# Optimization experiments

Measured on AMD Instinct MI355X. Metric: run time of the kernel, lower is better.

Reference implementation:

```python
import jax, jax.numpy as jnp
import numpy as np

SIGMA = 0.05
KSIZE = 3
MIN_VAL = 50.0
MAX_VAL = 100.0


def _gauss_kernel():
    # ax = range(-(3//2)+1, 3//2+1) = [-1, 0, 1]  (matches TF int-floor-div)
    ax = jnp.arange(-(KSIZE // 2) + 1.0, KSIZE // 2 + 1.0)
    xx, yy = jnp.meshgrid(ax, ax)
    k = jnp.exp(-(xx ** 2 + yy ** 2) / (2.0 * SIGMA ** 2))
    k = k / jnp.sum(k)
    return k[..., None, None].astype(jnp.float32)  # HWIO, C=1


def _reflect_pad(x):
    return jnp.pad(x, ((0, 0), (1, 1), (1, 1), (0, 0)), mode='reflect')


def _conv(x, k):
    return jax.lax.conv_general_dilated(x, k, (1, 1), 'VALID',
                                        dimension_numbers=('NHWC', 'HWIO', 'NHWC'))


def _canny(images):
    blur = _conv(_reflect_pad(images), _gauss_kernel())
    h = jnp.array([[-1, 0, 1], [-2, 0, 2], [-1, 0, 1]], jnp.float32)[..., None, None]
    v = jnp.array([[-1, -2, -1], [0, 0, 0], [1, 2, 1]], jnp.float32)[..., None, None]
    bp = _reflect_pad(blur)
    gx = _conv(bp, h)
    gy = _conv(bp, v)
    gxy = jnp.sqrt(gx ** 2 + gy ** 2)
    # NOTE: original uses atan2(gx, gy) in this arg order
    theta = (jnp.arctan2(gx, gy) * (180.0 / np.pi) + 90.0) % 180.0

    H, W = gx.shape[1], gx.shape[2]
    # dilation2d with a -inf/0 kernel == max over the kernel's zero-offsets of the
    # zero-padded image; offsets are (dy,dx) of the 0 entries of each 3x3 filter.
    offsets = [
        [(1, 0), (1, 1), (1, 2)],  # horizontal bin: middle row
        [(0, 2), (1, 1), (2, 0)],  # 45 deg: anti-diagonal
        [(0, 1), (1, 1), (2, 1)],  # vertical bin: middle column
        [(0, 0), (1, 1), (2, 2)],  # 135 deg: main diagonal
    ]
    conds = [
        jnp.logical_or(theta >= 157.5, theta < 22.5),
        jnp.logical_and(theta >= 22.5, theta < 67.5),
        jnp.logical_and(theta >= 67.5, theta < 112.5),
        jnp.logical_and(theta >= 112.5, theta < 157.5),
    ]

    edge = jnp.zeros_like(gxy)
    for cond, offs in zip(conds, offsets):
        ang = jnp.where(cond, gxy, 0.0)
        pad = jnp.pad(ang, ((0, 0), (1, 1), (1, 1), (0, 0)))  # zero pad, as ZeroPadding2D
        mp = pad[:, offs[0][0]:offs[0][0] + H, offs[0][1]:offs[0][1] + W, :]
        for dy, dx in offs[1:]:
            mp = jnp.maximum(mp, pad[:, dy:dy + H, dx:dx + W, :])
        edge = edge + jnp.where(mp == ang, ang, 0.0)

    edge_sure = jnp.where(edge >= MAX_VAL, 255.0, 0.0)
    edge_week = jnp.where(jnp.logical_and(edge >= MIN_VAL, edge < MAX_VAL), 255.0, 0.0)
    edge_image = jnp.where(jnp.logical_or(edge_week == 255.0, edge_sure == 255.0), 255.5, 0.0)
    return edge_image, edge_week, edge_sure


def setup_inputs() -> dict:
    key = jax.random.key(0)
    images = jax.random.uniform(key, (16, 1024, 1024, 1), dtype=jnp.float32) * 255.0
    return {"images": images}


def reference(images):
    return _canny(images)
```

## Files before the change

kernel.cpp:

```cpp
#include <hip/hip_runtime.h>
#include <math.h>

#define IMG_H 1024
#define IMG_W 1024
#define OUT_H 1025
#define OUT_W 1025
#define NIMG  16
#define TOTAL (NIMG * OUT_H * OUT_W)

#define TILE_W 64
#define TILE_H 16
#define HALO_W 68
#define HALO_H 18
#define NQX    17
#define NQUAD  (HALO_H * NQX)
#define NTHREADS 320

__device__ __forceinline__ int refl(int k) {
    if (k >= 2) return (k <= 1025) ? (k - 2) : 1022;
    return k;
}

__device__ __forceinline__ void sobel_generic(const float* __restrict__ img, int i, int j,
                                              float& gx, float& gy) {
    int r0 = refl(i), r1 = refl(i + 1), r2 = refl(i + 2);
    int c0 = refl(j), c1 = refl(j + 1), c2 = refl(j + 2);
    const float* p0 = img + r0 * IMG_W;
    const float* p1 = img + r1 * IMG_W;
    const float* p2 = img + r2 * IMG_W;
    float v00 = p0[c0], v01 = p0[c1], v02 = p0[c2];
    float v10 = p1[c0],               v12 = p1[c2];
    float v20 = p2[c0], v21 = p2[c1], v22 = p2[c2];

    float t = -v00;
    t = __fadd_rn(t, v02);
    t = __fadd_rn(t, -2.0f * v10);
    t = __fadd_rn(t, 2.0f * v12);
    t = __fadd_rn(t, -v20);
    gx = __fadd_rn(t, v22);

    t = -v00;
    t = __fadd_rn(t, -2.0f * v01);
    t = __fadd_rn(t, -v02);
    t = __fadd_rn(t, v20);
    t = __fadd_rn(t, 2.0f * v21);
    gy = __fadd_rn(t, v22);
}

__device__ int classify_slow(float gx, float gy) {
    float t = (float)atan2((double)gx, (double)gy);
    float deg = __fmul_rn(t, (float)(180.0 / M_PI));
    float th = __fadd_rn(deg, 90.0f);
    th = fmodf(th, 180.0f);
    if (th < 0.0f) th += 180.0f;
    if (th < 22.5f || th >= 157.5f) return 0;
    if (th < 67.5f) return 1;
    if (th < 112.5f) return 2;
    return 3;
}

__device__ __forceinline__ int classify(float gx, float gy) {
    float ax = fabsf(gx), ay = fabsf(gy);
    const float T22_LO = 0.414172141e0f;
    const float T22_HI = 0.414254984e0f;
    const float T67_LO = 2.413972141e0f;
    const float T67_HI = 2.414454984e0f;

    if (ax <= ay * T22_LO) return 2;
    if (ax >= ay * T67_HI) return 0;
    if (ax >= ay * T22_HI && ax <= ay * T67_LO) {
        unsigned s = (__float_as_uint(gx) ^ __float_as_uint(gy)) >> 31;
        return s ? 1 : 3;
    }
    return classify_slow(gx, gy);
}

__device__ __forceinline__ float mag(float gx, float gy) {
    return __fsqrt_rn(__fadd_rn(__fmul_rn(gx, gx), __fmul_rn(gy, gy)));
}

__device__ __forceinline__ void load6(const float* __restrict__ p, float v[6]) {
    float4 a = *(const float4*)p;
    float2 b = *(const float2*)(p + 4);
    v[0] = a.x; v[1] = a.y; v[2] = a.z; v[3] = a.w; v[4] = b.x; v[5] = b.y;
}

__global__ __launch_bounds__(NTHREADS) void canny_kernel(const float* __restrict__ images,
                                                         float* __restrict__ out) {
    __shared__ float    g_s[HALO_H * HALO_W];
    __shared__ unsigned b_u[HALO_H * NQX];

    const int tile_ox = blockIdx.x * TILE_W;
    const int tile_oy = blockIdx.y * TILE_H;
    const int n       = blockIdx.z;
    const float* img = images + (size_t)n * IMG_H * IMG_W;
    const int t = threadIdx.x;

    if (t < NQUAD) {
        int hy  = t / NQX;
        int qx  = t - hy * NQX;
        int oy  = tile_oy + hy - 1;
        int ox0 = tile_ox + qx * 4 - 2;

        float    gq[4];
        unsigned bq[4];

        if (oy >= 2 && oy <= 1023 && ox0 >= 2 && ox0 <= 1020) {
            const float* r0p = img + (oy - 2) * IMG_W + (ox0 - 2);
            float R0[6], R1[6], R2[6];
            load6(r0p, R0);
            load6(r0p + IMG_W, R1);
            load6(r0p + 2 * IMG_W, R2);
            #pragma unroll
            for (int p = 0; p < 4; p++) {
                float v00 = R0[p], v01 = R0[p + 1], v02 = R0[p + 2];
                float v10 = R1[p],                  v12 = R1[p + 2];
                float v20 = R2[p], v21 = R2[p + 1], v22 = R2[p + 2];

                float s = -v00;
                s = __fadd_rn(s, v02);
                s = __fadd_rn(s, -2.0f * v10);
                s = __fadd_rn(s, 2.0f * v12);
                s = __fadd_rn(s, -v20);
                float gx = __fadd_rn(s, v22);

                s = -v00;
                s = __fadd_rn(s, -2.0f * v01);
                s = __fadd_rn(s, -v02);
                s = __fadd_rn(s, v20);
                s = __fadd_rn(s, 2.0f * v21);
                float gy = __fadd_rn(s, v22);

                gq[p] = mag(gx, gy);
                bq[p] = (unsigned)classify(gx, gy);
            }
        } else {
            #pragma unroll
            for (int p = 0; p < 4; p++) {
                int ox = ox0 + p;
                float g = -1.0f;
                unsigned b = 255u;
                if (oy >= 0 && oy < OUT_H && ox >= 0 && ox < OUT_W) {
                    float gx, gy;
                    sobel_generic(img, oy, ox, gx, gy);
                    g = mag(gx, gy);
                    b = (unsigned)classify(gx, gy);
                }
                gq[p] = g;
                bq[p] = b;
            }
        }

        int ldoff = hy * HALO_W + qx * 4;
        *(float4*)&g_s[ldoff] = make_float4(gq[0], gq[1], gq[2], gq[3]);
        b_u[hy * NQX + qx] = bq[0] | (bq[1] << 8) | (bq[2] << 16) | (bq[3] << 24);
    }
    __syncthreads();

    const unsigned char* b_s = (const unsigned char*)b_u;
    #pragma unroll
    for (int q = 0; q < 4; q++) {
        int p = t + NTHREADS * q;
        if (p >= TILE_W * TILE_H) break;
        int r = p >> 6, c = p & 63;
        int oy = tile_oy + r, ox = tile_ox + c;
        if (oy >= OUT_H || ox >= OUT_W) continue;

        int hc = (r + 1) * HALO_W + (c + 2);
        float gc = g_s[hc];
        int   bc = b_s[hc];

        int doff = (bc == 0) ? 1
                 : (bc == 1) ? (HALO_W - 1)
                 : (bc == 2) ? HALO_W
                 :             (HALO_W + 1);

        float nmax = 0.0f;
        float g1 = g_s[hc + doff];
        if (b_s[hc + doff] == bc && g1 > nmax) nmax = g1;
        float g2 = g_s[hc - doff];
        if (b_s[hc - doff] == bc && g2 > nmax) nmax = g2;

        float e = (gc >= nmax) ? gc : 0.0f;

        size_t o = (size_t)(n * OUT_H + oy) * OUT_W + ox;
        out[o]                       = (e >= 50.0f) ? 255.5f : 0.0f;
        out[(size_t)TOTAL + o]       = (e >= 50.0f && e < 100.0f) ? 255.0f : 0.0f;
        out[(size_t)(2 * TOTAL) + o] = (e >= 100.0f) ? 255.0f : 0.0f;
    }
}

extern "C" void kernel_launch(void* const* d_in, const int* in_sizes, int n_in,
                              void* d_out, int out_size, void* d_ws, size_t ws_size,
                              hipStream_t stream) {
    const float* images = (const float*)d_in[0];
    float* out = (float*)d_out;
    dim3 grid((OUT_W + TILE_W - 1) / TILE_W,
              (OUT_H + TILE_H - 1) / TILE_H,
              NIMG);
    canny_kernel<<<grid, NTHREADS, 0, stream>>>(images, out);
}
```

Before: 301.7 us.

## Replace 2D tiles with per-wave vertical strip streaming and LDS ring buffer

Replaces the 2D tiled block (halo gradient computed into shared memory, then a block-wide sync) with a per-wavefront column strip that walks down a band of rows. Input rows are prefetched into registers, and gradient magnitude and direction bins go into a 4-row LDS ring buffer that is private to each wave. This removes the __syncthreads and the halo recomputation between vertically adjacent tiles. In exchange it adds a serial dependency along rows within each wave, uses narrower per-lane scalar loads instead of float4 loads, and has 2 of every 64 lanes doing halo-only work.

```diff
diff --git a/kernel.cpp b/kernel.cpp
--- a/kernel.cpp
+++ b/kernel.cpp
@@ -8,43 +8,24 @@
 #define NIMG  16
 #define TOTAL (NIMG * OUT_H * OUT_W)
 
-#define TILE_W 64
-#define TILE_H 16
-#define HALO_W 68
-#define HALO_H 18
-#define NQX    17
-#define NQUAD  (HALO_H * NQX)
-#define NTHREADS 320
+#define STRIPW   62
+#define NSTRIPS  17
+#define NBANDS   16
+#define BANDH    65
+#define WAVES_PER_BLOCK 4
+#define NTHREADS 256
+#define NWAVES  (NSTRIPS * NBANDS * NIMG)
+#define NBLOCKS (NWAVES / WAVES_PER_BLOCK)
 
-__device__ __forceinline__ int refl(int k) {
+#define GR_W 68
+#define LDS_PER_WAVE_DW (2 * 4 * GR_W)
+
+__device__ __forceinline__ int refl_idx(int k) {
     if (k >= 2) return (k <= 1025) ? (k - 2) : 1022;
     return k;
 }
-
-__device__ __forceinline__ void sobel_generic(const float* __restrict__ img, int i, int j,
-                                              float& gx, float& gy) {
-    int r0 = refl(i), r1 = refl(i + 1), r2 = refl(i + 2);
-    int c0 = refl(j), c1 = refl(j + 1), c2 = refl(j + 2);
-    const float* p0 = img + r0 * IMG_W;
-    const float* p1 = img + r1 * IMG_W;
-    const float* p2 = img + r2 * IMG_W;
-    float v00 = p0[c0], v01 = p0[c1], v02 = p0[c2];
-    float v10 = p1[c0],               v12 = p1[c2];
-    float v20 = p2[c0], v21 = p2[c1], v22 = p2[c2];
-
-    float t = -v00;
-    t = __fadd_rn(t, v02);
-    t = __fadd_rn(t, -2.0f * v10);
-    t = __fadd_rn(t, 2.0f * v12);
-    t = __fadd_rn(t, -v20);
-    gx = __fadd_rn(t, v22);
-
-    t = -v00;
-    t = __fadd_rn(t, -2.0f * v01);
-    t = __fadd_rn(t, -v02);
-    t = __fadd_rn(t, v20);
-    t = __fadd_rn(t, 2.0f * v21);
-    gy = __fadd_rn(t, v22);
+__device__ __forceinline__ int clamp0(int k, int hi) {
+    return k < 0 ? 0 : (k > hi ? hi : k);
 }
 
 __device__ int classify_slow(float gx, float gy) {
@@ -79,43 +60,66 @@
     return __fsqrt_rn(__fadd_rn(__fmul_rn(gx, gx), __fmul_rn(gy, gy)));
 }
 
-__device__ __forceinline__ void load6(const float* __restrict__ p, float v[6]) {
-    float4 a = *(const float4*)p;
-    float2 b = *(const float2*)(p + 4);
-    v[0] = a.x; v[1] = a.y; v[2] = a.z; v[3] = a.w; v[4] = b.x; v[5] = b.y;
-}
+__global__ __launch_bounds__(NTHREADS, 5) void canny_kernel(const float* __restrict__ images,
+                                                            float* __restrict__ out) {
+    __shared__ float lds[WAVES_PER_BLOCK * LDS_PER_WAVE_DW];
 
-__global__ __launch_bounds__(NTHREADS) void canny_kernel(const float* __restrict__ images,
-                                                         float* __restrict__ out) {
-    __shared__ float    g_s[HALO_H * HALO_W];
-    __shared__ unsigned b_u[HALO_H * NQX];
+    const int tid = threadIdx.x;
+    const int w   = tid >> 6;
+    const int L   = tid & 63;
 
-    const int tile_ox = blockIdx.x * TILE_W;
-    const int tile_oy = blockIdx.y * TILE_H;
-    const int n       = blockIdx.z;
-    const float* img = images + (size_t)n * IMG_H * IMG_W;
-    const int t = threadIdx.x;
+    const int gw    = blockIdx.x * WAVES_PER_BLOCK + w;
+    const int img_i = gw / (NSTRIPS * NBANDS);
+    const int rem   = gw - img_i * (NSTRIPS * NBANDS);
+    const int band  = rem / NSTRIPS;
+    const int strip = rem - band * NSTRIPS;
 
-    if (t < NQUAD) {
-        int hy  = t / NQX;
-        int qx  = t - hy * NQX;
-        int oy  = tile_oy + hy - 1;
-        int ox0 = tile_ox + qx * 4 - 2;
+    const float* img = images + (size_t)img_i * IMG_H * IMG_W;
 
-        float    gq[4];
-        unsigned bq[4];
+    const int col0 = strip * STRIPW;
+    const int c    = col0 - 1 + L;
+    const int mc0 = refl_idx(clamp0(c,     1026));
+    const int mc1 = refl_idx(clamp0(c + 1, 1026));
+    const int mc2 = refl_idx(clamp0(c + 2, 1026));
 
-        if (oy >= 2 && oy <= 1023 && ox0 >= 2 && ox0 <= 1020) {
-            const float* r0p = img + (oy - 2) * IMG_W + (ox0 - 2);
-            float R0[6], R1[6], R2[6];
-            load6(r0p, R0);
-            load6(r0p + IMG_W, R1);
-            load6(r0p + 2 * IMG_W, R2);
-            #pragma unroll
-            for (int p = 0; p < 4; p++) {
-                float v00 = R0[p], v01 = R0[p + 1], v02 = R0[p + 2];
-                float v10 = R1[p],                  v12 = R1[p + 2];
-                float v20 = R2[p], v21 = R2[p + 1], v22 = R2[p + 2];
+    const int ys = band * BANDH;
+    const int ye = min(ys + BANDH, OUT_H);
+    const int gs = max(ys - 1, 0);
+    const int ge = min(ye, 1024);
+    const int tmax = ye - gs;
+
+    float*    gring = lds + w * LDS_PER_WAVE_DW;
+    unsigned* bring = (unsigned*)(gring + 4 * GR_W);
+
+    const bool laneValid = (c >= 0 && c <= 1024);
+    const bool storeLane = (L >= 1 && L <= 62 && c <= 1024);
+
+    const float* __restrict__ imgr = img;
+    #define ROWPTR(k) (imgr + (size_t)refl_idx((k) > 1026 ? 1026 : (k)) * IMG_W)
+
+    const float* rp;
+    rp = ROWPTR(gs);     float T0a = rp[mc0], T0b = rp[mc1], T0c = rp[mc2];
+    rp = ROWPTR(gs + 1); float T1a = rp[mc0], T1b = rp[mc1], T1c = rp[mc2];
+    float Pa[4], Pb[4], Pc[4];
+    #pragma unroll
+    for (int j = 0; j < 4; ++j) {
+        rp = ROWPTR(gs + 2 + j);
+        Pa[j] = rp[mc0]; Pb[j] = rp[mc1]; Pc[j] = rp[mc2];
+    }
+    float prevG = 0.0f; unsigned prevB = 255u;
+
+    for (int t0 = 0; t0 <= tmax; t0 += 4) {
+        #pragma unroll
+        for (int j = 0; j < 4; ++j) {
+            const int t = t0 + j;
+            if (t > tmax) break;
+            const int i = gs + t;
+            float g = -1.0f; unsigned b = 255u;
+
+            if (i <= ge) {
+                float v20 = Pa[j], v21 = Pb[j], v22 = Pc[j];
+                float v00 = T0a,  v01 = T0b,  v02 = T0c;
+                float v10 = T1a,              v12 = T1c;
 
                 float s = -v00;
                 s = __fadd_rn(s, v02);
@@ -131,72 +135,60 @@
                 s = __fadd_rn(s, 2.0f * v21);
                 float gy = __fadd_rn(s, v22);
 
-                gq[p] = mag(gx, gy);
-                bq[p] = (unsigned)classify(gx, gy);
-            }
-        } else {
-            #pragma unroll
-            for (int p = 0; p < 4; p++) {
-                int ox = ox0 + p;
-                float g = -1.0f;
-                unsigned b = 255u;
-                if (oy >= 0 && oy < OUT_H && ox >= 0 && ox < OUT_W) {
-                    float gx, gy;
-                    sobel_generic(img, oy, ox, gx, gy);
+                if (laneValid) {
                     g = mag(gx, gy);
                     b = (unsigned)classify(gx, gy);
                 }
-                gq[p] = g;
-                bq[p] = b;
+
+                int slot = (i & 3) * GR_W + (L + 1);
+                gring[slot] = g;
+                bring[slot] = b;
+
+                T0a = T1a; T0b = T1b; T0c = T1c;
+                T1a = v20; T1b = v21; T1c = v22;
+            }
+
+            const int y = i - 1;
+            if (y >= ys && y < ye) {
+                float    gc = prevG;
+                unsigned bc = prevB;
+                int dy = (bc == 0u) ? 0 : 1;
+                int dx = (bc == 0u) ? 1 : (bc == 1u) ? -1 : (bc == 2u) ? 0 : 1;
+                int p1 = ((unsigned)(y + dy) & 3u) * GR_W + (L + 1 + dx);
+                int p2 = ((unsigned)(y - dy) & 3u) * GR_W + (L + 1 - dx);
+                float    n1g = gring[p1]; unsigned n1b = bring[p1];
+                float    n2g = gring[p2]; unsigned n2b = bring[p2];
+                bool v1 = (y + dy) <= 1024;
+                bool v2 = (y - dy) >= 0;
+                float nmax = 0.0f;
+                if (v1 && n1b == bc && n1g > nmax) nmax = n1g;
+                if (v2 && n2b == bc && n2g > nmax) nmax = n2g;
+                float e = (gc >= nmax) ? gc : 0.0f;
+
+                if (storeLane) {
+                    size_t o = (size_t)(img_i * OUT_H + y) * OUT_W + c;
+                    out[o]                         = (e >= 50.0f) ? 255.5f : 0.0f;
+                    out[(size_t)TOTAL + o]         = (e >= 50.0f && e < 100.0f) ? 255.0f : 0.0f;
+                    out[(size_t)(2 * TOTAL) + o]   = (e >= 100.0f) ? 255.0f : 0.0f;
+                }
+            }
+
+            if (i <= ge) { prevG = g; prevB = b; }
+
+            if (i + 6 <= ge + 2) {
+                rp = ROWPTR(i + 6);
+                Pa[j] = rp[mc0]; Pb[j] = rp[mc1]; Pc[j] = rp[mc2];
             }
         }
-
-        int ldoff = hy * HALO_W + qx * 4;
-        *(float4*)&g_s[ldoff] = make_float4(gq[0], gq[1], gq[2], gq[3]);
-        b_u[hy * NQX + qx] = bq[0] | (bq[1] << 8) | (bq[2] << 16) | (bq[3] << 24);
     }
-    __syncthreads();
-
-    const unsigned char* b_s = (const unsigned char*)b_u;
-    #pragma unroll
-    for (int q = 0; q < 4; q++) {
-        int p = t + NTHREADS * q;
-        if (p >= TILE_W * TILE_H) break;
-        int r = p >> 6, c = p & 63;
-        int oy = tile_oy + r, ox = tile_ox + c;
-        if (oy >= OUT_H || ox >= OUT_W) continue;
-
-        int hc = (r + 1) * HALO_W + (c + 2);
-        float gc = g_s[hc];
-        int   bc = b_s[hc];
-
-        int doff = (bc == 0) ? 1
-                 : (bc == 1) ? (HALO_W - 1)
-                 : (bc == 2) ? HALO_W
-                 :             (HALO_W + 1);
-
-        float nmax = 0.0f;
-        float g1 = g_s[hc + doff];
-        if (b_s[hc + doff] == bc && g1 > nmax) nmax = g1;
-        float g2 = g_s[hc - doff];
-        if (b_s[hc - doff] == bc && g2 > nmax) nmax = g2;
-
-        float e = (gc >= nmax) ? gc : 0.0f;
-
-        size_t o = (size_t)(n * OUT_H + oy) * OUT_W + ox;
-        out[o]                       = (e >= 50.0f) ? 255.5f : 0.0f;
-        out[(size_t)TOTAL + o]       = (e >= 50.0f && e < 100.0f) ? 255.0f : 0.0f;
-        out[(size_t)(2 * TOTAL) + o] = (e >= 100.0f) ? 255.0f : 0.0f;
-    }
+    #undef ROWPTR
 }
 
 extern "C" void kernel_launch(void* const* d_in, const int* in_sizes, int n_in,
                               void* d_out, int out_size, void* d_ws, size_t ws_size,
                               hipStream_t stream) {
     const float* images = (const float*)d_in[0];
-    float* out = (float*)d_out;
-    dim3 grid((OUT_W + TILE_W - 1) / TILE_W,
-              (OUT_H + TILE_H - 1) / TILE_H,
-              NIMG);
-    canny_kernel<<<grid, NTHREADS, 0, stream>>>(images, out);
+    float* outp = (float*)d_out;
+    dim3 grid(NBLOCKS, 1, 1);
+    canny_kernel<<<grid, NTHREADS, 0, stream>>>(images, outp);
 }
```

New measurement: 345.0 us. +14.4%, slower.

## Replace shared-memory tiles with per-wave row tasks computing halo in registers

Applied to the files above, without the earlier changes.

Drops the shared-memory tile and barrier. Each wavefront now handles a quarter of one output row, and each lane computes a 3x6 patch of gradients from a 5x12 register window so it can do non-max suppression without cross-thread exchange. The last output column is handled by separate edge tasks, and the slow atan2 fallback is marked noinline to keep register pressure down. This recomputes halo gradients about 4.5x per output pixel and uses many registers, in exchange for removing LDS traffic and synchronization. Output stores are now scalar and stride by 4 across lanes, so they are no longer fully coalesced.

```diff
diff --git a/kernel.cpp b/kernel.cpp
--- a/kernel.cpp
+++ b/kernel.cpp
@@ -8,13 +8,11 @@
 #define NIMG  16
 #define TOTAL (NIMG * OUT_H * OUT_W)
 
-#define TILE_W 64
-#define TILE_H 16
-#define HALO_W 68
-#define HALO_H 18
-#define NQX    17
-#define NQUAD  (HALO_H * NQX)
-#define NTHREADS 320
+#define NTHREADS   256
+#define ROW_TASKS  (OUT_H * 4)
+#define EDGE_TASKS 17
+#define NTASKS     (ROW_TASKS + EDGE_TASKS)
+#define NBLOCKS    ((NTASKS + 3) / 4)
 
 __device__ __forceinline__ int refl(int k) {
     if (k >= 2) return (k <= 1025) ? (k - 2) : 1022;
@@ -47,7 +45,7 @@
     gy = __fadd_rn(t, v22);
 }
 
-__device__ int classify_slow(float gx, float gy) {
+__device__ __attribute__((noinline)) int classify_slow(float gx, float gy) {
     float t = (float)atan2((double)gx, (double)gy);
     float deg = __fmul_rn(t, (float)(180.0 / M_PI));
     float th = __fadd_rn(deg, 90.0f);
@@ -79,114 +77,137 @@
     return __fsqrt_rn(__fadd_rn(__fmul_rn(gx, gx), __fmul_rn(gy, gy)));
 }
 
-__device__ __forceinline__ void load6(const float* __restrict__ p, float v[6]) {
-    float4 a = *(const float4*)p;
-    float2 b = *(const float2*)(p + 4);
-    v[0] = a.x; v[1] = a.y; v[2] = a.z; v[3] = a.w; v[4] = b.x; v[5] = b.y;
-}
-
-__global__ __launch_bounds__(NTHREADS) void canny_kernel(const float* __restrict__ images,
-                                                         float* __restrict__ out) {
-    __shared__ float    g_s[HALO_H * HALO_W];
-    __shared__ unsigned b_u[HALO_H * NQX];
-
-    const int tile_ox = blockIdx.x * TILE_W;
-    const int tile_oy = blockIdx.y * TILE_H;
-    const int n       = blockIdx.z;
-    const float* img = images + (size_t)n * IMG_H * IMG_W;
-    const int t = threadIdx.x;
-
-    if (t < NQUAD) {
-        int hy  = t / NQX;
-        int qx  = t - hy * NQX;
-        int oy  = tile_oy + hy - 1;
-        int ox0 = tile_ox + qx * 4 - 2;
-
-        float    gq[4];
-        unsigned bq[4];
-
-        if (oy >= 2 && oy <= 1023 && ox0 >= 2 && ox0 <= 1020) {
-            const float* r0p = img + (oy - 2) * IMG_W + (ox0 - 2);
-            float R0[6], R1[6], R2[6];
-            load6(r0p, R0);
-            load6(r0p + IMG_W, R1);
-            load6(r0p + 2 * IMG_W, R2);
+__device__ __forceinline__ void gb_at(const float* __restrict__ img, int y, int x,
+                                      float& g, unsigned& b) {
+    if (y >= 0 && y < OUT_H && x >= 0 && x < OUT_W) {
+        float gx, gy;
+        sobel_generic(img, y, x, gx, gy);
+        g = mag(gx, gy);
+        b = (unsigned)classify(gx, gy);
+    } else {
+        g = -1.0f;
+        b = 255u;
+    }
+}
+
+__device__ __forceinline__ float px_generic(const float* __restrict__ img, int y, int x) {
+    float gx, gy;
+    sobel_generic(img, y, x, gx, gy);
+    float    gc = mag(gx, gy);
+    unsigned bc = (unsigned)classify(gx, gy);
+    int dy = (bc == 0u) ? 0 : 1;
+    int dx = (bc == 0u) ? 1 : (bc == 1u) ? -1 : (bc == 2u) ? 0 : 1;
+    float n1g, n2g; unsigned n1b, n2b;
+    gb_at(img, y + dy, x + dx, n1g, n1b);
+    gb_at(img, y - dy, x - dx, n2g, n2b);
+    float nmax = 0.0f;
+    if (n1b == bc && n1g > nmax) nmax = n1g;
+    if (n2b == bc && n2g > nmax) nmax = n2g;
+    return (gc >= nmax) ? gc : 0.0f;
+}
+
+__device__ __forceinline__ void store_px(float* __restrict__ out, size_t o, float e) {
+    out[o]                       = (e >= 50.0f) ? 255.5f : 0.0f;
+    out[(size_t)TOTAL + o]       = (e >= 50.0f && e < 100.0f) ? 255.0f : 0.0f;
+    out[(size_t)(2 * TOTAL) + o] = (e >= 100.0f) ? 255.0f : 0.0f;
+}
+
+__global__ __launch_bounds__(NTHREADS, 4) void canny_kernel(const float* __restrict__ images,
+                                                            float* __restrict__ out) {
+    const int tid = threadIdx.x;
+    const int w   = tid >> 6;
+    const int L   = tid & 63;
+    const int id  = blockIdx.x * 4 + w;
+    if (id >= NTASKS) return;
+
+    const int img_i = blockIdx.y;
+    const float* img = images + (size_t)img_i * IMG_H * IMG_W;
+
+    if (id < ROW_TASKS) {
+        const int y   = id >> 2;
+        const int seg = id & 3;
+        const int j0  = seg * 256 + 4 * L;
+
+        float e0, e1, e2, e3;
+        const bool fast = (y >= 3 && y <= 1022 && j0 >= 4 && j0 <= 1016);
+        if (fast) {
+            float R[5][12];
             #pragma unroll
-            for (int p = 0; p < 4; p++) {
-                float v00 = R0[p], v01 = R0[p + 1], v02 = R0[p + 2];
-                float v10 = R1[p],                  v12 = R1[p + 2];
-                float v20 = R2[p], v21 = R2[p + 1], v22 = R2[p + 2];
-
-                float s = -v00;
-                s = __fadd_rn(s, v02);
-                s = __fadd_rn(s, -2.0f * v10);
-                s = __fadd_rn(s, 2.0f * v12);
-                s = __fadd_rn(s, -v20);
-                float gx = __fadd_rn(s, v22);
-
-                s = -v00;
-                s = __fadd_rn(s, -2.0f * v01);
-                s = __fadd_rn(s, -v02);
-                s = __fadd_rn(s, v20);
-                s = __fadd_rn(s, 2.0f * v21);
-                float gy = __fadd_rn(s, v22);
-
-                gq[p] = mag(gx, gy);
-                bq[p] = (unsigned)classify(gx, gy);
+            for (int r = 0; r < 5; ++r) {
+                const float* rp = img + (size_t)(y - 3 + r) * IMG_W + (j0 - 4);
+                *(float4*)&R[r][0] = *(const float4*)rp;
+                *(float4*)&R[r][4] = *(const float4*)(rp + 4);
+                *(float4*)&R[r][8] = *(const float4*)(rp + 8);
             }
+
+            float    G[3][6];
+            unsigned B[3][6];
+            #pragma unroll
+            for (int a = 0; a < 3; ++a) {
+                #pragma unroll
+                for (int u = 0; u < 6; ++u) {
+                    float v00 = R[a][u + 1],     v01 = R[a][u + 2],     v02 = R[a][u + 3];
+                    float v10 = R[a + 1][u + 1],                        v12 = R[a + 1][u + 3];
+                    float v20 = R[a + 2][u + 1], v21 = R[a + 2][u + 2], v22 = R[a + 2][u + 3];
+
+                    float s = -v00;
+                    s = __fadd_rn(s, v02);
+                    s = __fadd_rn(s, -2.0f * v10);
+                    s = __fadd_rn(s, 2.0f * v12);
+                    s = __fadd_rn(s, -v20);
+                    float gx = __fadd_rn(s, v22);
+
+                    s = -v00;
+                    s = __fadd_rn(s, -2.0f * v01);
+                    s = __fadd_rn(s, -v02);
+                    s = __fadd_rn(s, v20);
+                    s = __fadd_rn(s, 2.0f * v21);
+                    float gy = __fadd_rn(s, v22);
+
+                    G[a][u] = mag(gx, gy);
+                    B[a][u] = (unsigned)classify(gx, gy);
+                }
+            }
+
+            float ee[4];
+            #pragma unroll
+            for (int p = 0; p < 4; ++p) {
+                float    gc = G[1][p + 1];
+                unsigned bc = B[1][p + 1];
+                float    n1g = (bc == 0u) ? G[1][p + 2] : (bc == 1u) ? G[2][p]
+                             : (bc == 2u) ? G[2][p + 1] : G[2][p + 2];
+                unsigned n1b = (bc == 0u) ? B[1][p + 2] : (bc == 1u) ? B[2][p]
+                             : (bc == 2u) ? B[2][p + 1] : B[2][p + 2];
+                float    n2g = (bc == 0u) ? G[1][p]     : (bc == 1u) ? G[0][p + 2]
+                             : (bc == 2u) ? G[0][p + 1] : G[0][p];
+                unsigned n2b = (bc == 0u) ? B[1][p]     : (bc == 1u) ? B[0][p + 2]
+                             : (bc == 2u) ? B[0][p + 1] : B[0][p];
+                float nmax = 0.0f;
+                if (n1b == bc && n1g > nmax) nmax = n1g;
+                if (n2b == bc && n2g > nmax) nmax = n2g;
+                ee[p] = (gc >= nmax) ? gc : 0.0f;
+            }
+            e0 = ee[0]; e1 = ee[1]; e2 = ee[2]; e3 = ee[3];
         } else {
-            #pragma unroll
-            for (int p = 0; p < 4; p++) {
-                int ox = ox0 + p;
-                float g = -1.0f;
-                unsigned b = 255u;
-                if (oy >= 0 && oy < OUT_H && ox >= 0 && ox < OUT_W) {
-                    float gx, gy;
-                    sobel_generic(img, oy, ox, gx, gy);
-                    g = mag(gx, gy);
-                    b = (unsigned)classify(gx, gy);
-                }
-                gq[p] = g;
-                bq[p] = b;
-            }
+            e0 = px_generic(img, y, j0);
+            e1 = px_generic(img, y, j0 + 1);
+            e2 = px_generic(img, y, j0 + 2);
+            e3 = px_generic(img, y, j0 + 3);
         }
 
-        int ldoff = hy * HALO_W + qx * 4;
-        *(float4*)&g_s[ldoff] = make_float4(gq[0], gq[1], gq[2], gq[3]);
-        b_u[hy * NQX + qx] = bq[0] | (bq[1] << 8) | (bq[2] << 16) | (bq[3] << 24);
-    }
-    __syncthreads();
-
-    const unsigned char* b_s = (const unsigned char*)b_u;
-    #pragma unroll
-    for (int q = 0; q < 4; q++) {
-        int p = t + NTHREADS * q;
-        if (p >= TILE_W * TILE_H) break;
-        int r = p >> 6, c = p & 63;
-        int oy = tile_oy + r, ox = tile_ox + c;
-        if (oy >= OUT_H || ox >= OUT_W) continue;
-
-        int hc = (r + 1) * HALO_W + (c + 2);
-        float gc = g_s[hc];
-        int   bc = b_s[hc];
-
-        int doff = (bc == 0) ? 1
-                 : (bc == 1) ? (HALO_W - 1)
-                 : (bc == 2) ? HALO_W
-                 :             (HALO_W + 1);
-
-        float nmax = 0.0f;
-        float g1 = g_s[hc + doff];
-        if (b_s[hc + doff] == bc && g1 > nmax) nmax = g1;
-        float g2 = g_s[hc - doff];
-        if (b_s[hc - doff] == bc && g2 > nmax) nmax = g2;
-
-        float e = (gc >= nmax) ? gc : 0.0f;
-
-        size_t o = (size_t)(n * OUT_H + oy) * OUT_W + ox;
-        out[o]                       = (e >= 50.0f) ? 255.5f : 0.0f;
-        out[(size_t)TOTAL + o]       = (e >= 50.0f && e < 100.0f) ? 255.0f : 0.0f;
-        out[(size_t)(2 * TOTAL) + o] = (e >= 100.0f) ? 255.0f : 0.0f;
+        size_t o = ((size_t)(img_i * OUT_H + y)) * OUT_W + j0;
+        store_px(out, o,     e0);
+        store_px(out, o + 1, e1);
+        store_px(out, o + 2, e2);
+        store_px(out, o + 3, e3);
+    } else {
+        const int k = id - ROW_TASKS;
+        const int y = k * 64 + L;
+        if (y < OUT_H) {
+            float e = px_generic(img, y, 1024);
+            size_t o = ((size_t)(img_i * OUT_H + y)) * OUT_W + 1024;
+            store_px(out, o, e);
+        }
     }
 }
 
@@ -194,9 +215,7 @@
                               void* d_out, int out_size, void* d_ws, size_t ws_size,
                               hipStream_t stream) {
     const float* images = (const float*)d_in[0];
-    float* out = (float*)d_out;
-    dim3 grid((OUT_W + TILE_W - 1) / TILE_W,
-              (OUT_H + TILE_H - 1) / TILE_H,
-              NIMG);
-    canny_kernel<<<grid, NTHREADS, 0, stream>>>(images, out);
-}
+    float* outp = (float*)d_out;
+    dim3 grid(NBLOCKS, NIMG, 1);
+    canny_kernel<<<grid, NTHREADS, 0, stream>>>(images, outp);
+}
```

Result: slower. 371.0 us (+23.0%).

## Assign one tile per wavefront, drop block barrier, prefetch next loads

Applied to the files above, without the earlier changes.

Restructures the kernel so each 64-lane wavefront owns a whole tile, with four tiles per 256-thread block on a flat 1D grid, removing __syncthreads. Gradient loads for the next quad pass are prefetched into registers while the current pass computes. The atan2 fallback is marked noinline to reduce register pressure, and launch bounds request higher occupancy. Correctness relies on the wave executing in lockstep for its shared-memory exchange, and the prefetch buffers raise register use.

```diff
diff --git a/kernel.cpp b/kernel.cpp
--- a/kernel.cpp
+++ b/kernel.cpp
@@ -14,7 +14,13 @@
 #define HALO_H 18
 #define NQX    17
 #define NQUAD  (HALO_H * NQX)
-#define NTHREADS 320
+#define NPASS  5
+#define WPB    4
+#define NTHREADS 256
+#define XTILES 17
+#define YTILESN 65
+#define NTASKS (XTILES * YTILESN * NIMG)
+#define NBLOCKS (NTASKS / WPB)
 
 __device__ __forceinline__ int refl(int k) {
     if (k >= 2) return (k <= 1025) ? (k - 2) : 1022;
@@ -47,7 +53,7 @@
     gy = __fadd_rn(t, v22);
 }
 
-__device__ int classify_slow(float gx, float gy) {
+__device__ __attribute__((noinline)) int classify_slow(float gx, float gy) {
     float t = (float)atan2((double)gx, (double)gy);
     float deg = __fmul_rn(t, (float)(180.0 / M_PI));
     float th = __fadd_rn(deg, 90.0f);
@@ -85,108 +91,156 @@
     v[0] = a.x; v[1] = a.y; v[2] = a.z; v[3] = a.w; v[4] = b.x; v[5] = b.y;
 }
 
-__global__ __launch_bounds__(NTHREADS) void canny_kernel(const float* __restrict__ images,
-                                                         float* __restrict__ out) {
-    __shared__ float    g_s[HALO_H * HALO_W];
-    __shared__ unsigned b_u[HALO_H * NQX];
-
-    const int tile_ox = blockIdx.x * TILE_W;
-    const int tile_oy = blockIdx.y * TILE_H;
-    const int n       = blockIdx.z;
-    const float* img = images + (size_t)n * IMG_H * IMG_W;
-    const int t = threadIdx.x;
-
-    if (t < NQUAD) {
-        int hy  = t / NQX;
-        int qx  = t - hy * NQX;
-        int oy  = tile_oy + hy - 1;
-        int ox0 = tile_ox + qx * 4 - 2;
-
-        float    gq[4];
-        unsigned bq[4];
-
+__global__ __launch_bounds__(NTHREADS, 5) void canny_kernel(const float* __restrict__ images,
+                                                            float* __restrict__ out) {
+    __shared__ float    g_all[WPB][HALO_H * HALO_W];
+    __shared__ unsigned b_all[WPB][HALO_H * NQX];
+
+    const int tid = threadIdx.x;
+    const int w   = tid >> 6;
+    const int L   = tid & 63;
+
+    const int task  = blockIdx.x * WPB + w;
+    const int img_i = task / (XTILES * YTILESN);
+    const int rem   = task - img_i * (XTILES * YTILESN);
+    const int ty    = rem / XTILES;
+    const int tx    = rem - ty * XTILES;
+
+    const int tile_ox = tx * TILE_W;
+    const int tile_oy = ty * TILE_H;
+    const float* img = images + (size_t)img_i * IMG_H * IMG_W;
+
+    float*    g_s = g_all[w];
+    unsigned* b_u = b_all[w];
+
+    float A[3][6], Bf[3][6];
+
+    {
+        int q  = L;
+        int hy = q / NQX, qx = q - hy * NQX;
+        int oy = tile_oy + hy - 1, ox0 = tile_ox + qx * 4 - 2;
         if (oy >= 2 && oy <= 1023 && ox0 >= 2 && ox0 <= 1020) {
-            const float* r0p = img + (oy - 2) * IMG_W + (ox0 - 2);
-            float R0[6], R1[6], R2[6];
-            load6(r0p, R0);
-            load6(r0p + IMG_W, R1);
-            load6(r0p + 2 * IMG_W, R2);
+            const float* r0p = img + (size_t)(oy - 2) * IMG_W + (ox0 - 2);
+            load6(r0p,             A[0]);
+            load6(r0p + IMG_W,     A[1]);
+            load6(r0p + 2 * IMG_W, A[2]);
+        }
+    }
+
+    #pragma unroll
+    for (int p = 0; p < NPASS; ++p) {
+        if (p + 1 < NPASS) {
+            int q  = (p + 1) * 64 + L;
+            int hy = q / NQX, qx = q - hy * NQX;
+            int oy = tile_oy + hy - 1, ox0 = tile_ox + qx * 4 - 2;
+            if (q < NQUAD && oy >= 2 && oy <= 1023 && ox0 >= 2 && ox0 <= 1020) {
+                const float* r0p = img + (size_t)(oy - 2) * IMG_W + (ox0 - 2);
+                load6(r0p,             Bf[0]);
+                load6(r0p + IMG_W,     Bf[1]);
+                load6(r0p + 2 * IMG_W, Bf[2]);
+            }
+        }
+
+        int q = p * 64 + L;
+        if (q < NQUAD) {
+            int hy = q / NQX, qx = q - hy * NQX;
+            int oy = tile_oy + hy - 1, ox0 = tile_ox + qx * 4 - 2;
+
+            float    gxs[4], gys[4], gq[4];
+            unsigned bq[4];
+
+            if (oy >= 2 && oy <= 1023 && ox0 >= 2 && ox0 <= 1020) {
+                #pragma unroll
+                for (int pp = 0; pp < 4; ++pp) {
+                    float v00 = A[0][pp], v01 = A[0][pp + 1], v02 = A[0][pp + 2];
+                    float v10 = A[1][pp],                     v12 = A[1][pp + 2];
+                    float v20 = A[2][pp], v21 = A[2][pp + 1], v22 = A[2][pp + 2];
+
+                    float s = -v00;
+                    s = __fadd_rn(s, v02);
+                    s = __fadd_rn(s, -2.0f * v10);
+                    s = __fadd_rn(s, 2.0f * v12);
+                    s = __fadd_rn(s, -v20);
+                    float gx = __fadd_rn(s, v22);
+
+                    s = -v00;
+                    s = __fadd_rn(s, -2.0f * v01);
+                    s = __fadd_rn(s, -v02);
+                    s = __fadd_rn(s, v20);
+                    s = __fadd_rn(s, 2.0f * v21);
+                    float gy = __fadd_rn(s, v22);
+
+                    gxs[pp] = gx;
+                    gys[pp] = gy;
+                    gq[pp]  = mag(gx, gy);
+                }
+            } else {
+                #pragma unroll
+                for (int pp = 0; pp < 4; ++pp) {
+                    int ox = ox0 + pp;
+                    if (oy >= 0 && oy < OUT_H && ox >= 0 && ox < OUT_W) {
+                        float gx, gy;
+                        sobel_generic(img, oy, ox, gx, gy);
+                        gxs[pp] = gx;
+                        gys[pp] = gy;
+                        gq[pp]  = mag(gx, gy);
+                    } else {
+                        gxs[pp] = 0.0f;
+                        gys[pp] = 1.0f;
+                        gq[pp]  = -1.0f;
+                    }
+                }
+            }
+
             #pragma unroll
-            for (int p = 0; p < 4; p++) {
-                float v00 = R0[p], v01 = R0[p + 1], v02 = R0[p + 2];
-                float v10 = R1[p],                  v12 = R1[p + 2];
-                float v20 = R2[p], v21 = R2[p + 1], v22 = R2[p + 2];
-
-                float s = -v00;
-                s = __fadd_rn(s, v02);
-                s = __fadd_rn(s, -2.0f * v10);
-                s = __fadd_rn(s, 2.0f * v12);
-                s = __fadd_rn(s, -v20);
-                float gx = __fadd_rn(s, v22);
-
-                s = -v00;
-                s = __fadd_rn(s, -2.0f * v01);
-                s = __fadd_rn(s, -v02);
-                s = __fadd_rn(s, v20);
-                s = __fadd_rn(s, 2.0f * v21);
-                float gy = __fadd_rn(s, v22);
-
-                gq[p] = mag(gx, gy);
-                bq[p] = (unsigned)classify(gx, gy);
+            for (int pp = 0; pp < 4; ++pp) {
+                bq[pp] = (gq[pp] < 0.0f) ? 255u : (unsigned)classify(gxs[pp], gys[pp]);
             }
-        } else {
+
+            int ldoff = hy * HALO_W + qx * 4;
+            *(float4*)&g_s[ldoff] = make_float4(gq[0], gq[1], gq[2], gq[3]);
+            b_u[hy * NQX + qx] = bq[0] | (bq[1] << 8) | (bq[2] << 16) | (bq[3] << 24);
+        }
+
+        if (p + 1 < NPASS) {
             #pragma unroll
-            for (int p = 0; p < 4; p++) {
-                int ox = ox0 + p;
-                float g = -1.0f;
-                unsigned b = 255u;
-                if (oy >= 0 && oy < OUT_H && ox >= 0 && ox < OUT_W) {
-                    float gx, gy;
-                    sobel_generic(img, oy, ox, gx, gy);
-                    g = mag(gx, gy);
-                    b = (unsigned)classify(gx, gy);
-                }
-                gq[p] = g;
-                bq[p] = b;
-            }
-        }
-
-        int ldoff = hy * HALO_W + qx * 4;
-        *(float4*)&g_s[ldoff] = make_float4(gq[0], gq[1], gq[2], gq[3]);
-        b_u[hy * NQX + qx] = bq[0] | (bq[1] << 8) | (bq[2] << 16) | (bq[3] << 24);
-    }
-    __syncthreads();
+            for (int r = 0; r < 3; ++r)
+                #pragma unroll
+                for (int cc = 0; cc < 6; ++cc)
+                    A[r][cc] = Bf[r][cc];
+        }
+    }
 
     const unsigned char* b_s = (const unsigned char*)b_u;
-    #pragma unroll
-    for (int q = 0; q < 4; q++) {
-        int p = t + NTHREADS * q;
-        if (p >= TILE_W * TILE_H) break;
-        int r = p >> 6, c = p & 63;
-        int oy = tile_oy + r, ox = tile_ox + c;
-        if (oy >= OUT_H || ox >= OUT_W) continue;
-
-        int hc = (r + 1) * HALO_W + (c + 2);
-        float gc = g_s[hc];
-        int   bc = b_s[hc];
-
-        int doff = (bc == 0) ? 1
-                 : (bc == 1) ? (HALO_W - 1)
-                 : (bc == 2) ? HALO_W
-                 :             (HALO_W + 1);
-
-        float nmax = 0.0f;
-        float g1 = g_s[hc + doff];
-        if (b_s[hc + doff] == bc && g1 > nmax) nmax = g1;
-        float g2 = g_s[hc - doff];
-        if (b_s[hc - doff] == bc && g2 > nmax) nmax = g2;
-
-        float e = (gc >= nmax) ? gc : 0.0f;
-
-        size_t o = (size_t)(n * OUT_H + oy) * OUT_W + ox;
-        out[o]                       = (e >= 50.0f) ? 255.5f : 0.0f;
-        out[(size_t)TOTAL + o]       = (e >= 50.0f && e < 100.0f) ? 255.0f : 0.0f;
-        out[(size_t)(2 * TOTAL) + o] = (e >= 100.0f) ? 255.0f : 0.0f;
+    const int ox = tile_ox + L;
+    if (ox < OUT_W) {
+        #pragma unroll 4
+        for (int k = 0; k < TILE_H; ++k) {
+            int oy = tile_oy + k;
+            if (oy >= OUT_H) break;
+
+            int hc = (k + 1) * HALO_W + (L + 2);
+            float gc = g_s[hc];
+            int   bc = b_s[hc];
+
+            int doff = (bc == 0) ? 1
+                     : (bc == 1) ? (HALO_W - 1)
+                     : (bc == 2) ? HALO_W
+                     :             (HALO_W + 1);
+
+            float nmax = 0.0f;
+            float g1 = g_s[hc + doff];
+            if (b_s[hc + doff] == bc && g1 > nmax) nmax = g1;
+            float g2 = g_s[hc - doff];
+            if (b_s[hc - doff] == bc && g2 > nmax) nmax = g2;
+
+            float e = (gc >= nmax) ? gc : 0.0f;
+
+            size_t o = (size_t)(img_i * OUT_H + oy) * OUT_W + ox;
+            out[o]                       = (e >= 50.0f) ? 255.5f : 0.0f;
+            out[(size_t)TOTAL + o]       = (e >= 50.0f && e < 100.0f) ? 255.0f : 0.0f;
+            out[(size_t)(2 * TOTAL) + o] = (e >= 100.0f) ? 255.0f : 0.0f;
+        }
     }
 }
 
@@ -194,9 +248,7 @@
                               void* d_out, int out_size, void* d_ws, size_t ws_size,
                               hipStream_t stream) {
     const float* images = (const float*)d_in[0];
-    float* out = (float*)d_out;
-    dim3 grid((OUT_W + TILE_W - 1) / TILE_W,
-              (OUT_H + TILE_H - 1) / TILE_H,
-              NIMG);
-    canny_kernel<<<grid, NTHREADS, 0, stream>>>(images, out);
-}
+    float* outp = (float*)d_out;
+    dim3 grid(NBLOCKS, 1, 1);
+    canny_kernel<<<grid, NTHREADS, 0, stream>>>(images, outp);
+}
```

Result: slower. 328.0 us (+8.7%).
